# Kernel tuning notes

Hardware: AMD Instinct MI355X
Metric: run time of the kernel (lower is better)

Reference implementation:

```python
import jax, jax.numpy as jnp
import numpy as np

T = 65536      # total tokens (flattened ragged batch)
H = 1024       # hidden size
B = 64         # number of segments (documents)
L = 2          # num_labels
EPS = 1e-12    # electra layer_norm_eps


def setup_inputs() -> dict:
    key = jax.random.key(0)
    k1, k2, k3, k4, k5, k6 = jax.random.split(key, 6)
    # ragged segment ids: sorted random ids in [0, B) covering all segments
    rng = np.random.default_rng(0)
    cuts = np.sort(rng.choice(np.arange(1, T), size=B - 1, replace=False))
    lengths = np.diff(np.concatenate([[0], cuts, [T]]))  # B positive lengths summing to T
    segment_ids = jnp.asarray(np.repeat(np.arange(B), lengths), dtype=jnp.int32)
    return {
        "sequence_attention_embeddings": jax.random.normal(k1, (T, H), dtype=jnp.float32),
        "sequence_embeddings": jax.random.normal(k2, (T, H), dtype=jnp.float32),
        "W_dense": jax.random.normal(k3, (H, H), dtype=jnp.float32) / np.sqrt(H),
        "b_dense": jnp.zeros((H,), dtype=jnp.float32),
        "gamma": jnp.ones((H,), dtype=jnp.float32),
        "beta": jnp.zeros((H,), dtype=jnp.float32),
        "W_out": jax.random.normal(k4, (H, L), dtype=jnp.float32) / np.sqrt(H),
        "b_out": jnp.zeros((L,), dtype=jnp.float32),
        "segment_ids": segment_ids,
    }


def reference(sequence_attention_embeddings, sequence_embeddings, W_dense, b_dense,
              gamma, beta, W_out, b_out, segment_ids):
    # dense projection on flattened tokens [T, H]
    h = sequence_attention_embeddings @ W_dense + b_dense
    # dropout is identity in eval mode
    # residual + LayerNorm
    h = h + sequence_embeddings
    mu = jnp.mean(h, axis=-1, keepdims=True)
    var = jnp.mean(jnp.square(h - mu), axis=-1, keepdims=True)
    h = (h - mu) / jnp.sqrt(var + EPS) * gamma + beta
    # ragged split + per-segment mean == fused segment mean
    sums = jax.ops.segment_sum(h, segment_ids, num_segments=B)          # [B, H]
    counts = jax.ops.segment_sum(jnp.ones((h.shape[0],), h.dtype), segment_ids, num_segments=B)
    agg = sums / counts[:, None]
    # final projection to logits [B, L]
    return agg @ W_out + b_out
```

## Files before the change

### kernel.cpp

```cpp
#include <hip/hip_runtime.h>

#define T_TOK 65536
#define HDIM  1024
#define NSEG  64

typedef _Float16 half8  __attribute__((ext_vector_type(8)));
typedef float    f32x4  __attribute__((ext_vector_type(4)));
typedef float    f32x16 __attribute__((ext_vector_type(16)));

#define WT_OFF   0ull
#define U0_OFF   2097152ull
#define U1_OFF   (U0_OFF + 4096ull)
#define CON_OFF  (U1_OFF + 4096ull)
#define ACC_OFF  (CON_OFF + 64ull)
#define CNT_OFF  (ACC_OFF + 512ull)

__global__ void prep_kernel(const float* __restrict__ gamma, const float* __restrict__ beta,
                            const float* __restrict__ wout, const int* __restrict__ segids,
                            float* __restrict__ u0, float* __restrict__ u1,
                            float* __restrict__ consts, float* __restrict__ segacc,
                            int* __restrict__ counts) {
    __shared__ int   starts[65];
    __shared__ float cacc[4];
    int tid = threadIdx.x;
    if (tid < 128) segacc[tid] = 0.f;
    if (tid < 4)   cacc[tid]   = 0.f;
    if (tid == 0) { starts[0] = 0; starts[64] = T_TOK; }
    __syncthreads();

    float g  = gamma[tid], be = beta[tid];
    float w0 = wout[2 * tid], w1 = wout[2 * tid + 1];
    float a0 = g * w0, a1 = g * w1;
    u0[tid] = a0; u1[tid] = a1;
    float v[4] = {a0, a1, be * w0, be * w1};
#pragma unroll
    for (int q = 0; q < 4; ++q) {
        float x = v[q];
#pragma unroll
        for (int off = 32; off > 0; off >>= 1) x += __shfl_down(x, off, 64);
        if ((tid & 63) == 0) atomicAdd(&cacc[q], x);
    }
    for (int i = tid; i < T_TOK - 1; i += 1024) {
        int s0 = segids[i], s1 = segids[i + 1];
        if (s1 != s0) starts[s1] = i + 1;
    }
    __syncthreads();
    if (tid < 64) counts[tid] = starts[tid + 1] - starts[tid];
    if (tid < 4)  consts[tid] = cacc[tid];
}

__global__ void wconv_kernel(const float* __restrict__ W, _Float16* __restrict__ Wt) {
    __shared__ float tile[64][65];
    int bx = blockIdx.x & 15;
    int by = blockIdx.x >> 4;
    int c0 = bx * 64, k0 = by * 64;
    int t  = threadIdx.x;
    int kk = t >> 6, cc = t & 63;
#pragma unroll
    for (int i = 0; i < 16; ++i) {
        int kl = kk * 16 + i;
        tile[cc][kl] = W[(size_t)(k0 + kl) * HDIM + c0 + cc];
    }
    __syncthreads();
#pragma unroll
    for (int i = 0; i < 16; ++i) {
        int cl = kk * 16 + i;
        Wt[(size_t)(c0 + cl) * HDIM + k0 + cc] = (_Float16)tile[cl][cc];
    }
}

#define A_LDS 33280

__global__ __launch_bounds__(512, 2) void gemm_kernel(
    const float* __restrict__ A, const float* __restrict__ R,
    const float* __restrict__ bdense, const _Float16* __restrict__ Wt,
    const float* __restrict__ u0g, const float* __restrict__ u1g,
    const float* __restrict__ consts, const int* __restrict__ segids,
    float* __restrict__ segacc) {
    __shared__ __align__(16) char smem[A_LDS + 512 + 256];
    int tid  = threadIdx.x;
    int lane = tid & 63, wave = tid >> 6;
    int ln = lane & 31, lh = lane >> 5;
    int rowBase = blockIdx.x * 64;
    int colB    = wave * 128;

    f32x16 acc[2][4];
#pragma unroll
    for (int tr = 0; tr < 2; ++tr)
#pragma unroll
        for (int tc = 0; tc < 4; ++tc)
#pragma unroll
            for (int i = 0; i < 16; ++i) acc[tr][tc][i] = 0.f;

    const _Float16* bq[4];
#pragma unroll
    for (int tc = 0; tc < 4; ++tc)
        bq[tc] = Wt + (size_t)(colB + tc * 32 + ln) * HDIM + lh * 8;

    int mloc0 = tid >> 5;
    int khalf = tid & 31;

    for (int kq = 0; kq < 4; ++kq) {
        __syncthreads();
#pragma unroll
        for (int i = 0; i < 4; ++i) {
            int mloc = mloc0 + i * 16;
            const float* src = A + (size_t)(rowBase + mloc) * HDIM + kq * 256 + khalf * 8;
            f32x4 a0 = *(const f32x4*)src;
            f32x4 a1 = *(const f32x4*)(src + 4);
            half8 s;
            s[0] = (_Float16)a0[0]; s[1] = (_Float16)a0[1];
            s[2] = (_Float16)a0[2]; s[3] = (_Float16)a0[3];
            s[4] = (_Float16)a1[0]; s[5] = (_Float16)a1[1];
            s[6] = (_Float16)a1[2]; s[7] = (_Float16)a1[3];
            *(half8*)(smem + khalf * 1040 + mloc * 16) = s;
        }
        __syncthreads();
#pragma unroll
        for (int ks = 0; ks < 16; ++ks) {
            half8 afr[2], bfr[4];
#pragma unroll
            for (int tr = 0; tr < 2; ++tr)
                afr[tr] = *(const half8*)(smem + (ks * 2 + lh) * 1040 + (tr * 32 + ln) * 16);
#pragma unroll
            for (int tc = 0; tc < 4; ++tc)
                bfr[tc] = *(const half8*)(bq[tc] + kq * 256 + ks * 16);
#pragma unroll
            for (int tr = 0; tr < 2; ++tr)
#pragma unroll
                for (int tc = 0; tc < 4; ++tc)
                    acc[tr][tc] = __builtin_amdgcn_mfma_f32_32x32x16_f16(
                        afr[tr], bfr[tc], acc[tr][tc], 0, 0, 0);
        }
    }

    __syncthreads();
    float* red  = (float*)smem;
#pragma unroll
    for (int i = 0; i < 16; ++i) red[tid + i * 512] = 0.f;
    float* sval = (float*)(smem + A_LDS);
    int*   sseg = (int*)(smem + A_LDS + 512);
    __syncthreads();

    float bv[4], u0v[4], u1v[4];
#pragma unroll
    for (int tc = 0; tc < 4; ++tc) {
        int c = colB + tc * 32 + ln;
        bv[tc] = bdense[c]; u0v[tc] = u0g[c]; u1v[tc] = u1g[c];
    }
#pragma unroll
    for (int tr = 0; tr < 2; ++tr)
#pragma unroll
        for (int reg = 0; reg < 16; ++reg) {
            int rIT   = (reg & 3) + 8 * (reg >> 2) + 4 * lh;
            int row64 = tr * 32 + rIT;
            size_t grow = (size_t)(rowBase + row64);
            float s1 = 0.f, s2 = 0.f, p0 = 0.f, p1 = 0.f;
#pragma unroll
            for (int tc = 0; tc < 4; ++tc) {
                float h = acc[tr][tc][reg] + bv[tc] + R[grow * HDIM + colB + tc * 32 + ln];
                s1 += h; s2 += h * h; p0 += h * u0v[tc]; p1 += h * u1v[tc];
            }
            atomicAdd(&red[row64 * 32 + ln], s1);
            atomicAdd(&red[2048 + row64 * 32 + ln], s2);
            atomicAdd(&red[4096 + row64 * 32 + ln], p0);
            atomicAdd(&red[6144 + row64 * 32 + ln], p1);
        }
    __syncthreads();
    if (tid < 64) {
        float s1 = 0.f, s2 = 0.f, p0 = 0.f, p1 = 0.f;
        for (int c = 0; c < 32; ++c) {
            s1 += red[tid * 32 + c];
            s2 += red[2048 + tid * 32 + c];
            p0 += red[4096 + tid * 32 + c];
            p1 += red[6144 + tid * 32 + c];
        }
        float mu  = s1 * (1.f / 1024.f);
        float var = s2 * (1.f / 1024.f) - mu * mu;
        float rsd = rsqrtf(var + 1e-12f);
        sval[tid * 2]     = rsd * (p0 - mu * consts[0]) + consts[2];
        sval[tid * 2 + 1] = rsd * (p1 - mu * consts[1]) + consts[3];
        sseg[tid] = segids[rowBase + tid];
    }
    __syncthreads();
    if (tid < 64) {
        int s = sseg[tid];
        if (tid == 63 || sseg[tid + 1] != s) {
            float a0 = 0.f, a1 = 0.f;
            int rr = tid;
            while (rr >= 0 && sseg[rr] == s) { a0 += sval[rr * 2]; a1 += sval[rr * 2 + 1]; --rr; }
            atomicAdd(&segacc[s * 2],     a0);
            atomicAdd(&segacc[s * 2 + 1], a1);
        }
    }
}

__global__ void finalize_kernel(const float* __restrict__ segacc, const int* __restrict__ counts,
                                const float* __restrict__ bout, float* __restrict__ out) {
    int t = threadIdx.x;
    if (t < 128) {
        int s = t >> 1, l = t & 1;
        out[t] = segacc[t] / (float)counts[s] + bout[l];
    }
}

extern "C" void kernel_launch(void* const* d_in, const int* in_sizes, int n_in,
                              void* d_out, int out_size, void* d_ws, size_t ws_size,
                              hipStream_t stream) {
    const float* A      = (const float*)d_in[0];
    const float* R      = (const float*)d_in[1];
    const float* Wd     = (const float*)d_in[2];
    const float* bdense = (const float*)d_in[3];
    const float* gamma  = (const float*)d_in[4];
    const float* beta   = (const float*)d_in[5];
    const float* wout   = (const float*)d_in[6];
    const float* bout   = (const float*)d_in[7];
    const int*   segids = (const int*)d_in[8];
    float* out = (float*)d_out;

    char* ws = (char*)d_ws;
    _Float16* Wt  = (_Float16*)(ws + WT_OFF);
    float* u0     = (float*)(ws + U0_OFF);
    float* u1     = (float*)(ws + U1_OFF);
    float* consts = (float*)(ws + CON_OFF);
    float* segacc = (float*)(ws + ACC_OFF);
    int*   counts = (int*)(ws + CNT_OFF);

    prep_kernel<<<1, 1024, 0, stream>>>(gamma, beta, wout, segids, u0, u1, consts, segacc, counts);
    wconv_kernel<<<256, 256, 0, stream>>>(Wd, Wt);
    gemm_kernel<<<1024, 512, 0, stream>>>(A, R, bdense, Wt, u0, u1, consts, segids, segacc);
    finalize_kernel<<<1, 128, 0, stream>>>(segacc, counts, bout, out);
}
```

Before: 1.055 ms.

## Pre-pack W into MFMA fragment order and use 16 waves per block

The weight conversion kernel now writes W in a packed layout in which each wave's B fragments for one k-step sit contiguously, so the per-lane B loads in the GEMM become fully coalesced 1 KB reads. The GEMM block grows to 1024 threads with each wave covering 64 columns instead of 128, which halves the accumulator registers per wave and adds parallelism for latency hiding. The per-row LayerNorm reduction is rewritten to use all threads with shuffle reductions instead of 64 serial threads. The risks are lower per-wave reuse of A fragments and more block-wide synchronisation cost with 16 waves.

New measurement: 1.241 ms. 1.18x slower.

```diff
diff --git a/kernel.cpp b/kernel.cpp
--- a/kernel.cpp
+++ b/kernel.cpp
@@ -5,10 +5,11 @@
 #define NSEG  64
 
 typedef _Float16 half8  __attribute__((ext_vector_type(8)));
+typedef float    f32x2  __attribute__((ext_vector_type(2)));
 typedef float    f32x4  __attribute__((ext_vector_type(4)));
 typedef float    f32x16 __attribute__((ext_vector_type(16)));
 
-#define WT_OFF   0ull
+#define WP_OFF   0ull
 #define U0_OFF   2097152ull
 #define U1_OFF   (U0_OFF + 4096ull)
 #define CON_OFF  (U1_OFF + 4096ull)
@@ -49,7 +50,7 @@
     if (tid < 4)  consts[tid] = cacc[tid];
 }
 
-__global__ void wconv_kernel(const float* __restrict__ W, _Float16* __restrict__ Wt) {
+__global__ void wpack_kernel(const float* __restrict__ W, _Float16* __restrict__ Wp) {
     __shared__ float tile[64][65];
     int bx = blockIdx.x & 15;
     int by = blockIdx.x >> 4;
@@ -59,21 +60,30 @@
 #pragma unroll
     for (int i = 0; i < 16; ++i) {
         int kl = kk * 16 + i;
-        tile[cc][kl] = W[(size_t)(k0 + kl) * HDIM + c0 + cc];
-    }
-    __syncthreads();
-#pragma unroll
-    for (int i = 0; i < 16; ++i) {
-        int cl = kk * 16 + i;
-        Wt[(size_t)(c0 + cl) * HDIM + k0 + cc] = (_Float16)tile[cl][cc];
+        tile[kl][cc] = W[(size_t)(k0 + kl) * HDIM + c0 + cc];
+    }
+    __syncthreads();
+    int cti  = t >> 7;
+    int ksgi = (t >> 5) & 3;
+    int ln   = t & 31;
+    int ct   = (c0 >> 5) + cti;
+    int ksg  = (k0 >> 4) + ksgi;
+#pragma unroll
+    for (int lh = 0; lh < 2; ++lh) {
+        int l = lh * 32 + ln;
+        half8 v;
+#pragma unroll
+        for (int j = 0; j < 8; ++j)
+            v[j] = (_Float16)tile[ksgi * 16 + lh * 8 + j][cti * 32 + ln];
+        *(half8*)(Wp + ((size_t)(ct * 64 + ksg) * 64 + l) * 8) = v;
     }
 }
 
 #define A_LDS 33280
 
-__global__ __launch_bounds__(512, 2) void gemm_kernel(
+__global__ __launch_bounds__(1024, 4) void gemm_kernel(
     const float* __restrict__ A, const float* __restrict__ R,
-    const float* __restrict__ bdense, const _Float16* __restrict__ Wt,
+    const float* __restrict__ bdense, const _Float16* __restrict__ Wp,
     const float* __restrict__ u0g, const float* __restrict__ u1g,
     const float* __restrict__ consts, const int* __restrict__ segids,
     float* __restrict__ segacc) {
@@ -82,29 +92,29 @@
     int lane = tid & 63, wave = tid >> 6;
     int ln = lane & 31, lh = lane >> 5;
     int rowBase = blockIdx.x * 64;
-    int colB    = wave * 128;
-
-    f32x16 acc[2][4];
+    int colW    = wave * 64;
+
+    f32x16 acc[2][2];
 #pragma unroll
     for (int tr = 0; tr < 2; ++tr)
 #pragma unroll
-        for (int tc = 0; tc < 4; ++tc)
+        for (int tc = 0; tc < 2; ++tc)
 #pragma unroll
             for (int i = 0; i < 16; ++i) acc[tr][tc][i] = 0.f;
 
-    const _Float16* bq[4];
-#pragma unroll
-    for (int tc = 0; tc < 4; ++tc)
-        bq[tc] = Wt + (size_t)(colB + tc * 32 + ln) * HDIM + lh * 8;
-
+    const _Float16* bp[2];
+#pragma unroll
+    for (int tc = 0; tc < 2; ++tc)
+        bp[tc] = Wp + ((size_t)(wave * 2 + tc) * 64 * 64 + lane) * 8;
+
+    int khalf = tid & 31;
     int mloc0 = tid >> 5;
-    int khalf = tid & 31;
 
     for (int kq = 0; kq < 4; ++kq) {
         __syncthreads();
 #pragma unroll
-        for (int i = 0; i < 4; ++i) {
-            int mloc = mloc0 + i * 16;
+        for (int i = 0; i < 2; ++i) {
+            int mloc = mloc0 + i * 32;
             const float* src = A + (size_t)(rowBase + mloc) * HDIM + kq * 256 + khalf * 8;
             f32x4 a0 = *(const f32x4*)src;
             f32x4 a1 = *(const f32x4*)(src + 4);
@@ -118,17 +128,18 @@
         __syncthreads();
 #pragma unroll
         for (int ks = 0; ks < 16; ++ks) {
-            half8 afr[2], bfr[4];
+            int ksg = kq * 16 + ks;
+            half8 afr[2], bfr[2];
+#pragma unroll
+            for (int tc = 0; tc < 2; ++tc)
+                bfr[tc] = *(const half8*)(bp[tc] + (size_t)ksg * 512);
 #pragma unroll
             for (int tr = 0; tr < 2; ++tr)
                 afr[tr] = *(const half8*)(smem + (ks * 2 + lh) * 1040 + (tr * 32 + ln) * 16);
 #pragma unroll
-            for (int tc = 0; tc < 4; ++tc)
-                bfr[tc] = *(const half8*)(bq[tc] + kq * 256 + ks * 16);
-#pragma unroll
             for (int tr = 0; tr < 2; ++tr)
 #pragma unroll
-                for (int tc = 0; tc < 4; ++tc)
+                for (int tc = 0; tc < 2; ++tc)
                     acc[tr][tc] = __builtin_amdgcn_mfma_f32_32x32x16_f16(
                         afr[tr], bfr[tc], acc[tr][tc], 0, 0, 0);
         }
@@ -137,15 +148,15 @@
     __syncthreads();
     float* red  = (float*)smem;
 #pragma unroll
-    for (int i = 0; i < 16; ++i) red[tid + i * 512] = 0.f;
+    for (int i = 0; i < 8; ++i) red[tid + i * 1024] = 0.f;
     float* sval = (float*)(smem + A_LDS);
     int*   sseg = (int*)(smem + A_LDS + 512);
     __syncthreads();
 
-    float bv[4], u0v[4], u1v[4];
-#pragma unroll
-    for (int tc = 0; tc < 4; ++tc) {
-        int c = colB + tc * 32 + ln;
+    float bv[2], u0v[2], u1v[2];
+#pragma unroll
+    for (int tc = 0; tc < 2; ++tc) {
+        int c = colW + tc * 32 + ln;
         bv[tc] = bdense[c]; u0v[tc] = u0g[c]; u1v[tc] = u1g[c];
     }
 #pragma unroll
@@ -157,8 +168,8 @@
             size_t grow = (size_t)(rowBase + row64);
             float s1 = 0.f, s2 = 0.f, p0 = 0.f, p1 = 0.f;
 #pragma unroll
-            for (int tc = 0; tc < 4; ++tc) {
-                float h = acc[tr][tc][reg] + bv[tc] + R[grow * HDIM + colB + tc * 32 + ln];
+            for (int tc = 0; tc < 2; ++tc) {
+                float h = acc[tr][tc][reg] + bv[tc] + R[grow * HDIM + colW + tc * 32 + ln];
                 s1 += h; s2 += h * h; p0 += h * u0v[tc]; p1 += h * u1v[tc];
             }
             atomicAdd(&red[row64 * 32 + ln], s1);
@@ -167,20 +178,30 @@
             atomicAdd(&red[6144 + row64 * 32 + ln], p1);
         }
     __syncthreads();
-    if (tid < 64) {
-        float s1 = 0.f, s2 = 0.f, p0 = 0.f, p1 = 0.f;
-        for (int c = 0; c < 32; ++c) {
-            s1 += red[tid * 32 + c];
-            s2 += red[2048 + tid * 32 + c];
-            p0 += red[4096 + tid * 32 + c];
-            p1 += red[6144 + tid * 32 + c];
-        }
-        float mu  = s1 * (1.f / 1024.f);
-        float var = s2 * (1.f / 1024.f) - mu * mu;
-        float rsd = rsqrtf(var + 1e-12f);
-        sval[tid * 2]     = rsd * (p0 - mu * consts[0]) + consts[2];
-        sval[tid * 2 + 1] = rsd * (p1 - mu * consts[1]) + consts[3];
-        sseg[tid] = segids[rowBase + tid];
+    {
+        int r = tid >> 4, i = tid & 15;
+        int j = (i + r) & 15;
+        f32x2 v0 = *(f32x2*)&red[r * 32 + 2 * j];
+        f32x2 v1 = *(f32x2*)&red[2048 + r * 32 + 2 * j];
+        f32x2 v2 = *(f32x2*)&red[4096 + r * 32 + 2 * j];
+        f32x2 v3 = *(f32x2*)&red[6144 + r * 32 + 2 * j];
+        float s1 = v0[0] + v0[1], s2 = v1[0] + v1[1];
+        float p0 = v2[0] + v2[1], p1 = v3[0] + v3[1];
+#pragma unroll
+        for (int off = 1; off < 16; off <<= 1) {
+            s1 += __shfl_xor(s1, off, 64);
+            s2 += __shfl_xor(s2, off, 64);
+            p0 += __shfl_xor(p0, off, 64);
+            p1 += __shfl_xor(p1, off, 64);
+        }
+        if (i == 0) {
+            float mu  = s1 * (1.f / 1024.f);
+            float var = s2 * (1.f / 1024.f) - mu * mu;
+            float rsd = rsqrtf(var + 1e-12f);
+            sval[r * 2]     = rsd * (p0 - mu * consts[0]) + consts[2];
+            sval[r * 2 + 1] = rsd * (p1 - mu * consts[1]) + consts[3];
+            sseg[r] = segids[rowBase + r];
+        }
     }
     __syncthreads();
     if (tid < 64) {
@@ -219,7 +240,7 @@
     float* out = (float*)d_out;
 
     char* ws = (char*)d_ws;
-    _Float16* Wt  = (_Float16*)(ws + WT_OFF);
+    _Float16* Wp  = (_Float16*)(ws + WP_OFF);
     float* u0     = (float*)(ws + U0_OFF);
     float* u1     = (float*)(ws + U1_OFF);
     float* consts = (float*)(ws + CON_OFF);
@@ -227,7 +248,7 @@
     int*   counts = (int*)(ws + CNT_OFF);
 
     prep_kernel<<<1, 1024, 0, stream>>>(gamma, beta, wout, segids, u0, u1, consts, segacc, counts);
-    wconv_kernel<<<256, 256, 0, stream>>>(Wd, Wt);
-    gemm_kernel<<<1024, 512, 0, stream>>>(A, R, bdense, Wt, u0, u1, consts, segids, segacc);
+    wpack_kernel<<<256, 256, 0, stream>>>(Wd, Wp);
+    gemm_kernel<<<1024, 1024, 0, stream>>>(A, R, bdense, Wp, u0, u1, consts, segids, segacc);
     finalize_kernel<<<1, 128, 0, stream>>>(segacc, counts, bout, out);
 }
```
